# Performance work log

Measured on AMD Instinct MI355X. Metric: run time of the kernel, lower is better.

The kernel has to match this reference:

```python
import jax, jax.numpy as jnp
import numpy as np

IN_CH = 64
INTER = IN_CH // 2
B, H, W = 2, 80, 80


def setup_inputs() -> dict:
    key = jax.random.key(0)
    k = jax.random.split(key, 5)
    s = 1.0 / np.sqrt(IN_CH)
    return {
        "x": jax.random.normal(k[0], (B, IN_CH, H, W), dtype=jnp.float32),
        "g_w": jax.random.normal(k[1], (INTER, IN_CH), dtype=jnp.float32) * s,
        "theta_w": jax.random.normal(k[2], (INTER, IN_CH), dtype=jnp.float32) * s,
        "phi_w": jax.random.normal(k[3], (INTER, IN_CH), dtype=jnp.float32) * s,
        "w_w": jax.random.normal(k[4], (IN_CH, INTER), dtype=jnp.float32) * (1.0 / np.sqrt(INTER)),
    }


def reference(x, g_w, theta_w, phi_w, w_w):
    # Non-local block: 1x1 convs (bias=False) are channel matmuls over N=H*W positions.
    Bc, C, Hh, Ww = x.shape
    N = Hh * Ww
    xf = x.reshape(Bc, C, N)                            # [B, C, N]
    g = jnp.einsum('ic,bcn->bni', g_w, xf)              # [B, N, inter]
    theta = jnp.einsum('ic,bcn->bni', theta_w, xf)      # [B, N, inter]
    phi = jnp.einsum('ic,bcn->bin', phi_w, xf)          # [B, inter, N]
    affinity = jax.nn.softmax(jnp.einsum('bni,bim->bnm', theta, phi), axis=-1)  # [B, N, N]
    y = jnp.einsum('bnm,bmi->bni', affinity, g)         # [B, N, inter]
    y = jnp.einsum('ci,bni->bcn', w_w, y).reshape(Bc, C, Hh, Ww)
    return x + y
```

## Files before the change

kernel.cpp:

```cpp
#include <hip/hip_runtime.h>
#include <math.h>

#define BATCH 2
#define CH    64
#define INTER 32
#define NPOS  6400
#define LOG2E 1.44269504088896f
#define SPLIT 10
#define TPB   5

typedef _Float16 f16x8 __attribute__((ext_vector_type(8)));
typedef _Float16 f16x2 __attribute__((ext_vector_type(2)));
typedef _Float16 h4    __attribute__((ext_vector_type(4)));
typedef float    f32x4 __attribute__((ext_vector_type(4)));

static __device__ __forceinline__ f16x2 pkrtz(float a, float b) {
    return __builtin_bit_cast(f16x2, __builtin_amdgcn_cvt_pkrtz(a, b));
}

__global__ __launch_bounds__(256) void nlb_proj_kernel(
    const float* __restrict__ x,
    const float* __restrict__ g_w,
    const float* __restrict__ th_w,
    const float* __restrict__ ph_w,
    _Float16* __restrict__ Qh, _Float16* __restrict__ Kh,
    _Float16* __restrict__ Vt)
{
    const int b  = blockIdx.z;
    const int p  = blockIdx.y;
    const int n0 = blockIdx.x * 64;
    const int t  = threadIdx.x;
    const int w  = __builtin_amdgcn_readfirstlane(t) >> 6;
    const int lane = t & 63;

    const float* wsrc = (p == 0) ? th_w : (p == 1) ? ph_w : g_w;
    const float* xg = x + (size_t)b * CH * NPOS + n0 + lane;

    float xr[64];
    #pragma unroll
    for (int c = 0; c < 64; c++) xr[c] = xg[(size_t)c * NPOS];

    __shared__ float buf[32][65];

    float accs[8];
    #pragma unroll
    for (int rr = 0; rr < 8; rr++) {
        const int row = w * 8 + rr;
        const float* wr = wsrc + row * 64;
        float a0 = 0.f, a1 = 0.f, a2 = 0.f, a3 = 0.f;
        #pragma unroll
        for (int c = 0; c < 16; c++) {
            a0 += wr[c]      * xr[c];
            a1 += wr[c + 16] * xr[c + 16];
            a2 += wr[c + 32] * xr[c + 32];
            a3 += wr[c + 48] * xr[c + 48];
        }
        accs[rr] = (a0 + a1) + (a2 + a3);
    }

    if (p == 2) {
        const int n   = n0 + lane;
        const int kk  = n & 127;
        const int g   = kk >> 4, qd = (kk >> 2) & 3, rr2 = kk & 3;
        const int slot = (g >> 1) * 32 + qd * 8 + (g & 1) * 4 + rr2;
        const size_t col = (size_t)(n >> 7) * 128 + slot;
        #pragma unroll
        for (int rr = 0; rr < 8; rr++)
            Vt[((size_t)b * 32 + w * 8 + rr) * NPOS + col] = (_Float16)accs[rr];
        return;
    }

    #pragma unroll
    for (int rr = 0; rr < 8; rr++) buf[w * 8 + rr][lane] = accs[rr];
    __syncthreads();

    const float scale = (p == 0) ? LOG2E : 1.f;
    _Float16* dst = (p == 0) ? Qh : Kh;
    const int pos = t >> 2, ic = t & 3;
    f16x8 hv;
    #pragma unroll
    for (int j = 0; j < 8; j++)
        hv[j] = (_Float16)(buf[ic * 8 + j][pos] * scale);
    *(f16x8*)(dst + ((size_t)b * NPOS + n0 + pos) * 32 + ic * 8) = hv;
}

__global__ __launch_bounds__(256) void nlb_flash_kernel(
    const _Float16* __restrict__ Qh, const _Float16* __restrict__ Kh,
    const _Float16* __restrict__ Vt,
    _Float16* __restrict__ Opart, float2* __restrict__ ml)
{
    __shared__ __align__(16) _Float16 ks[128][40];
    __shared__ __align__(16) _Float16 vs[32][136];

    const int b     = blockIdx.z;
    const int split = blockIdx.y;
    const int t     = threadIdx.x;
    const int w     = t >> 6;
    const int lane  = t & 63;
    const int n16   = lane & 15;
    const int quad  = lane >> 4;
    const int q0    = blockIdx.x * 64 + w * 16;

    const f16x8 qa = *(const f16x8*)(Qh + ((size_t)b * NPOS + q0 + n16) * 32 + quad * 8);

    const _Float16* KB = Kh + (size_t)b * NPOS * 32;
    const _Float16* VB = Vt + (size_t)b * 32 * NPOS;

    f32x4 o0 = (f32x4)0.f;
    f32x4 o1 = (f32x4)0.f;
    float runm = -1e30f, lsum = 0.f;

    const int key0 = t >> 2, part = t & 3, key1 = key0 + 64;
    const int dim0 = t >> 4, kp   = t & 15, dim1 = dim0 + 16;

    const int kt0 = split * TPB;
    f16x8 kr0, kr1, vr0, vr1;
    {
        const int k0 = kt0 * 128;
        kr0 = *(const f16x8*)(KB + (size_t)(k0 + key0) * 32 + part * 8);
        kr1 = *(const f16x8*)(KB + (size_t)(k0 + key1) * 32 + part * 8);
        vr0 = *(const f16x8*)(VB + (size_t)dim0 * NPOS + k0 + kp * 8);
        vr1 = *(const f16x8*)(VB + (size_t)dim1 * NPOS + k0 + kp * 8);
    }

    for (int i = 0; i < TPB; i++) {
        if (i) __syncthreads();
        *(f16x8*)&ks[key0][part * 8] = kr0;
        *(f16x8*)&ks[key1][part * 8] = kr1;
        *(f16x8*)&vs[dim0][kp * 8]   = vr0;
        *(f16x8*)&vs[dim1][kp * 8]   = vr1;
        __syncthreads();

        if (i + 1 < TPB) {
            const int k0n = (kt0 + i + 1) * 128;
            kr0 = *(const f16x8*)(KB + (size_t)(k0n + key0) * 32 + part * 8);
            kr1 = *(const f16x8*)(KB + (size_t)(k0n + key1) * 32 + part * 8);
            vr0 = *(const f16x8*)(VB + (size_t)dim0 * NPOS + k0n + kp * 8);
            vr1 = *(const f16x8*)(VB + (size_t)dim1 * NPOS + k0n + kp * 8);
        }

        f32x4 sc[8];
        #pragma unroll
        for (int g = 0; g < 8; g++) {
            f16x8 kf = *(const f16x8*)&ks[g * 16 + n16][quad * 8];
            f32x4 z = (f32x4)0.f;
            sc[g] = __builtin_amdgcn_mfma_f32_16x16x32_f16(kf, qa, z, 0, 0, 0);
        }

        float m = fmaxf(fmaxf(sc[0][0], sc[0][1]), fmaxf(sc[0][2], sc[0][3]));
        #pragma unroll
        for (int g = 1; g < 8; g++) {
            float mg = fmaxf(fmaxf(sc[g][0], sc[g][1]), fmaxf(sc[g][2], sc[g][3]));
            m = fmaxf(m, mg);
        }
        m = fmaxf(m, __shfl_xor(m, 16));
        m = fmaxf(m, __shfl_xor(m, 32));
        float nm = fmaxf(runm, m);
        float a  = __builtin_amdgcn_exp2f(runm - nm);
        runm = nm;
        float ls = 0.f;
        #pragma unroll
        for (int g = 0; g < 8; g++) {
            #pragma unroll
            for (int r = 0; r < 4; r++) {
                float p = __builtin_amdgcn_exp2f(sc[g][r] - nm);
                sc[g][r] = p;
                ls += p;
            }
        }
        lsum = lsum * a + ls;
        o0 *= a;
        o1 *= a;

        #pragma unroll
        for (int kc = 0; kc < 4; kc++) {
            union { f16x8 v; f16x2 h2[4]; } pb;
            pb.h2[0] = pkrtz(sc[kc * 2][0],     sc[kc * 2][1]);
            pb.h2[1] = pkrtz(sc[kc * 2][2],     sc[kc * 2][3]);
            pb.h2[2] = pkrtz(sc[kc * 2 + 1][0], sc[kc * 2 + 1][1]);
            pb.h2[3] = pkrtz(sc[kc * 2 + 1][2], sc[kc * 2 + 1][3]);
            f16x8 v0 = *(const f16x8*)&vs[n16][kc * 32 + quad * 8];
            f16x8 v1 = *(const f16x8*)&vs[16 + n16][kc * 32 + quad * 8];
            o0 = __builtin_amdgcn_mfma_f32_16x16x32_f16(v0, pb.v, o0, 0, 0, 0);
            o1 = __builtin_amdgcn_mfma_f32_16x16x32_f16(v1, pb.v, o1, 0, 0, 0);
        }
    }

    lsum += __shfl_xor(lsum, 16);
    lsum += __shfl_xor(lsum, 32);
    float invl = 1.f / lsum;
    const size_t base = ((size_t)(b * SPLIT + split) * NPOS + q0 + n16) * 32;
    h4 h0, h1;
    #pragma unroll
    for (int r = 0; r < 4; r++) {
        h0[r] = (_Float16)(o0[r] * invl);
        h1[r] = (_Float16)(o1[r] * invl);
    }
    *(h4*)(Opart + base + quad * 4)      = h0;
    *(h4*)(Opart + base + 16 + quad * 4) = h1;
    if (quad == 0)
        ml[(size_t)(b * SPLIT + split) * NPOS + q0 + n16] = make_float2(runm, lsum);
}

__global__ __launch_bounds__(256) void nlb_combine_kernel(
    const _Float16* __restrict__ Opart, const float2* __restrict__ ml,
    const float* __restrict__ w_w, const float* __restrict__ x,
    float* __restrict__ out)
{
    __shared__ float wf[64][33];
    __shared__ float wts[32][12];
    __shared__ float of[32][33];

    const int b  = blockIdx.y;
    const int q0 = blockIdx.x * 32;
    const int t  = threadIdx.x;

    for (int idx = t; idx < 2048; idx += 256) wf[idx >> 5][idx & 31] = w_w[idx];

    if (t < 32) {
        float2 v[SPLIT];
        float m = -1e30f;
        #pragma unroll
        for (int s = 0; s < SPLIT; s++) {
            v[s] = ml[(size_t)(b * SPLIT + s) * NPOS + q0 + t];
            m = fmaxf(m, v[s].x);
        }
        float suml = 0.f;
        #pragma unroll
        for (int s = 0; s < SPLIT; s++) {
            float wgt = __builtin_amdgcn_exp2f(v[s].x - m) * v[s].y;
            wts[t][s] = wgt;
            suml += wgt;
        }
        float inv = 1.f / suml;
        #pragma unroll
        for (int s = 0; s < SPLIT; s++) wts[t][s] *= inv;
    }
    __syncthreads();

    {
        const int q = t >> 3, dg = t & 7;
        float a0 = 0.f, a1 = 0.f, a2 = 0.f, a3 = 0.f;
        #pragma unroll
        for (int s = 0; s < SPLIT; s++) {
            h4 hv = *(const h4*)(Opart +
                ((size_t)(b * SPLIT + s) * NPOS + q0 + q) * 32 + dg * 4);
            float c = wts[q][s];
            a0 += c * (float)hv[0]; a1 += c * (float)hv[1];
            a2 += c * (float)hv[2]; a3 += c * (float)hv[3];
        }
        of[q][dg * 4]     = a0; of[q][dg * 4 + 1] = a1;
        of[q][dg * 4 + 2] = a2; of[q][dg * 4 + 3] = a3;
    }
    __syncthreads();

    {
        const int q = t & 31, cg = t >> 5;
        const float* xb = x   + (size_t)b * CH * NPOS + q0 + q;
        float*       ob = out + (size_t)b * CH * NPOS + q0 + q;
        #pragma unroll
        for (int cc = 0; cc < 8; cc++) {
            int ch = cg * 8 + cc;
            float acc = 0.f;
            #pragma unroll
            for (int i = 0; i < 32; i++) acc += wf[ch][i] * of[q][i];
            ob[(size_t)ch * NPOS] = acc + xb[(size_t)ch * NPOS];
        }
    }
}

extern "C" void kernel_launch(void* const* d_in, const int* in_sizes, int n_in,
                              void* d_out, int out_size, void* d_ws, size_t ws_size,
                              hipStream_t stream) {
    const float* x    = (const float*)d_in[0];
    const float* g_w  = (const float*)d_in[1];
    const float* th_w = (const float*)d_in[2];
    const float* ph_w = (const float*)d_in[3];
    const float* w_w  = (const float*)d_in[4];
    float* out = (float*)d_out;

    const size_t SZ = (size_t)BATCH * NPOS * INTER;
    _Float16* Qh = (_Float16*)d_ws;
    _Float16* Kh = Qh + SZ;
    _Float16* Vt = Kh + SZ;
    _Float16* Opart = Vt + SZ;
    float2*   ml    = (float2*)(Opart + SZ * SPLIT);

    nlb_proj_kernel<<<dim3(NPOS / 64, 3, BATCH), 256, 0, stream>>>(
        x, g_w, th_w, ph_w, Qh, Kh, Vt);
    nlb_flash_kernel<<<dim3(NPOS / 64, SPLIT, BATCH), 256, 0, stream>>>(
        Qh, Kh, Vt, Opart, ml);
    nlb_combine_kernel<<<dim3(NPOS / 32, BATCH), 256, 0, stream>>>(
        Opart, ml, w_w, x, out);
}
```

Before: 107.4 us.

## Load K/V MFMA fragments directly from global memory, dropping LDS staging

The flash kernel no longer stages K and V tiles in shared memory. Each wave now loads its MFMA operand fragments for K and V straight from global memory into registers, which removes the block-wide barriers and the LDS write/read traffic. In exchange, all four waves of a block fetch the same K/V data from global memory or L2 instead of sharing it, and the register prefetch of the next tile is gone. Latency must now be hidden by occupancy rather than by explicit double-buffering.

```diff
diff --git a/kernel.cpp b/kernel.cpp
--- a/kernel.cpp
+++ b/kernel.cpp
@@ -89,9 +89,6 @@
     const _Float16* __restrict__ Vt,
     _Float16* __restrict__ Opart, float2* __restrict__ ml)
 {
-    __shared__ __align__(16) _Float16 ks[128][40];
-    __shared__ __align__(16) _Float16 vs[32][136];
-
     const int b     = blockIdx.z;
     const int split = blockIdx.y;
     const int t     = threadIdx.x;
@@ -103,48 +100,35 @@
 
     const f16x8 qa = *(const f16x8*)(Qh + ((size_t)b * NPOS + q0 + n16) * 32 + quad * 8);
 
-    const _Float16* KB = Kh + (size_t)b * NPOS * 32;
-    const _Float16* VB = Vt + (size_t)b * 32 * NPOS;
+    const _Float16* kp = Kh + (size_t)b * NPOS * 32 + (size_t)n16 * 32 + quad * 8;
+    const _Float16* vp = Vt + ((size_t)b * 32 + n16) * NPOS + quad * 8;
 
     f32x4 o0 = (f32x4)0.f;
     f32x4 o1 = (f32x4)0.f;
     float runm = -1e30f, lsum = 0.f;
 
-    const int key0 = t >> 2, part = t & 3, key1 = key0 + 64;
-    const int dim0 = t >> 4, kp   = t & 15, dim1 = dim0 + 16;
-
-    const int kt0 = split * TPB;
-    f16x8 kr0, kr1, vr0, vr1;
-    {
-        const int k0 = kt0 * 128;
-        kr0 = *(const f16x8*)(KB + (size_t)(k0 + key0) * 32 + part * 8);
-        kr1 = *(const f16x8*)(KB + (size_t)(k0 + key1) * 32 + part * 8);
-        vr0 = *(const f16x8*)(VB + (size_t)dim0 * NPOS + k0 + kp * 8);
-        vr1 = *(const f16x8*)(VB + (size_t)dim1 * NPOS + k0 + kp * 8);
-    }
+    const int k0base = split * TPB * 128;
 
     for (int i = 0; i < TPB; i++) {
-        if (i) __syncthreads();
-        *(f16x8*)&ks[key0][part * 8] = kr0;
-        *(f16x8*)&ks[key1][part * 8] = kr1;
-        *(f16x8*)&vs[dim0][kp * 8]   = vr0;
-        *(f16x8*)&vs[dim1][kp * 8]   = vr1;
-        __syncthreads();
-
-        if (i + 1 < TPB) {
-            const int k0n = (kt0 + i + 1) * 128;
-            kr0 = *(const f16x8*)(KB + (size_t)(k0n + key0) * 32 + part * 8);
-            kr1 = *(const f16x8*)(KB + (size_t)(k0n + key1) * 32 + part * 8);
-            vr0 = *(const f16x8*)(VB + (size_t)dim0 * NPOS + k0n + kp * 8);
-            vr1 = *(const f16x8*)(VB + (size_t)dim1 * NPOS + k0n + kp * 8);
-        }
+        const int k0 = k0base + i * 128;
+
+        f16x8 kr[8];
+        #pragma unroll
+        for (int g = 0; g < 8; g++)
+            kr[g] = *(const f16x8*)(kp + (size_t)(k0 + g * 16) * 32);
 
         f32x4 sc[8];
         #pragma unroll
         for (int g = 0; g < 8; g++) {
-            f16x8 kf = *(const f16x8*)&ks[g * 16 + n16][quad * 8];
             f32x4 z = (f32x4)0.f;
-            sc[g] = __builtin_amdgcn_mfma_f32_16x16x32_f16(kf, qa, z, 0, 0, 0);
+            sc[g] = __builtin_amdgcn_mfma_f32_16x16x32_f16(kr[g], qa, z, 0, 0, 0);
+        }
+
+        f16x8 vr0[4], vr1[4];
+        #pragma unroll
+        for (int kc = 0; kc < 4; kc++) {
+            vr0[kc] = *(const f16x8*)(vp + k0 + kc * 32);
+            vr1[kc] = *(const f16x8*)(vp + (size_t)16 * NPOS + k0 + kc * 32);
         }
 
         float m = fmaxf(fmaxf(sc[0][0], sc[0][1]), fmaxf(sc[0][2], sc[0][3]));
@@ -179,10 +163,8 @@
             pb.h2[1] = pkrtz(sc[kc * 2][2],     sc[kc * 2][3]);
             pb.h2[2] = pkrtz(sc[kc * 2 + 1][0], sc[kc * 2 + 1][1]);
             pb.h2[3] = pkrtz(sc[kc * 2 + 1][2], sc[kc * 2 + 1][3]);
-            f16x8 v0 = *(const f16x8*)&vs[n16][kc * 32 + quad * 8];
-            f16x8 v1 = *(const f16x8*)&vs[16 + n16][kc * 32 + quad * 8];
-            o0 = __builtin_amdgcn_mfma_f32_16x16x32_f16(v0, pb.v, o0, 0, 0, 0);
-            o1 = __builtin_amdgcn_mfma_f32_16x16x32_f16(v1, pb.v, o1, 0, 0, 0);
+            o0 = __builtin_amdgcn_mfma_f32_16x16x32_f16(vr0[kc], pb.v, o0, 0, 0, 0);
+            o1 = __builtin_amdgcn_mfma_f32_16x16x32_f16(vr1[kc], pb.v, o1, 0, 0, 0);
         }
     }
 
```

New measurement: 137.1 us. 27.7% more time.
